# Kernel optimization log

Measured on AMD Instinct MI355X. Metric: run time of the kernel, lower is better.

## Reference

```python
import jax, jax.numpy as jnp
import numpy as np

K_NEIGHBOURS = 40  # includes self; self is dropped after top-k


def setup_inputs() -> dict:
    key = jax.random.key(0)
    ks = jax.random.split(key, 4)
    B, V, F_in = 4, 4096, 64
    P, S, F_out = 64, 4, 64
    x = jax.random.normal(ks[0], (B, V, F_in), dtype=jnp.float32)
    Wf = jax.random.normal(ks[1], (F_in, P), dtype=jnp.float32) / np.sqrt(F_in)
    bf = jnp.zeros((P,), dtype=jnp.float32)
    Ws = jax.random.normal(ks[2], (F_in, S), dtype=jnp.float32) / np.sqrt(F_in)
    bs = jnp.zeros((S,), dtype=jnp.float32)
    Wo = jax.random.normal(ks[3], (F_in + 2 * P, F_out), dtype=jnp.float32) / np.sqrt(F_in + 2 * P)
    bo = jnpp = jnp.zeros((F_out,), dtype=jnp.float32)
    return {"x": x, "Wf": Wf, "bf": bf, "Ws": Ws, "bs": bs, "Wo": Wo, "bo": bo}


def _euclidean_squared(c):
    # c: [B, V, S] -> [B, V, V] squared pairwise distances
    sq = jnp.sum(c * c, axis=-1)  # [B, V]
    d2 = sq[:, :, None] + sq[:, None, :] - 2.0 * jnp.einsum('bvs,bus->bvu', c, c)
    return d2


def reference(x, Wf, bf, Ws, bs, Wo, bo):
    # learned spatial coordinates and propagated features
    coords = x @ Ws + bs            # [B, V, S]
    feats = x @ Wf + bf             # [B, V, P]

    d2 = _euclidean_squared(coords)                 # [B, V, V]
    neg_vals, idx = jax.lax.top_k(-d2, K_NEIGHBOURS)  # closest first (self at 0)
    nbr_idx = idx[:, :, 1:]                         # [B, V, K-1]
    dist = -neg_vals[:, :, 1:]                      # [B, V, K-1] (>= 0)

    # gauss_of_lin(d * 10) = exp(-|10 d|)
    w = jnp.exp(-jnp.abs(dist * 10.0))              # [B, V, K-1]

    # gather neighbour features per batch: [B, V, K-1, P]
    nf = jax.vmap(lambda f, i: f[i])(feats, nbr_idx)
    nf = nf * w[..., None]

    collected = jnp.concatenate([jnp.max(nf, axis=2), jnp.mean(nf, axis=2)], axis=-1)  # [B, V, 2P]
    updated = jnp.concatenate([x, collected], axis=-1)  # [B, V, F_in + 2P]
    return jnp.tanh(updated @ Wo + bo)
```

## Files before the change

### kernel.cpp

```cpp
#include <hip/hip_runtime.h>
#include <cmath>

#define BB  4
#define VV  4096
#define KK  40
#define FIN 64

typedef float v2f __attribute__((ext_vector_type(2)));

__global__ __launch_bounds__(256) void prep_kernel(
    const float* __restrict__ x, const float* __restrict__ Wf,
    const float* __restrict__ bf, const float* __restrict__ Ws,
    const float* __restrict__ bs,
    float* __restrict__ coords, float* __restrict__ sq,
    float* __restrict__ feats)
{
    int lane = threadIdx.x & 63;
    int wid  = threadIdx.x >> 6;
    int row0 = (blockIdx.x * 4 + wid) * 4;
    const float* xr = x + (size_t)row0 * FIN;

    float a0 = 0.f, a1 = 0.f, a2 = 0.f, a3 = 0.f;
    #pragma unroll 8
    for (int k = 0; k < FIN; ++k) {
        float wf = Wf[k * 64 + lane];
        a0 = fmaf(xr[k],        wf, a0);
        a1 = fmaf(xr[64  + k],  wf, a1);
        a2 = fmaf(xr[128 + k],  wf, a2);
        a3 = fmaf(xr[192 + k],  wf, a3);
    }
    float bfl = bf[lane];
    feats[(size_t)(row0 + 0) * 64 + lane] = a0 + bfl;
    feats[(size_t)(row0 + 1) * 64 + lane] = a1 + bfl;
    feats[(size_t)(row0 + 2) * 64 + lane] = a2 + bfl;
    feats[(size_t)(row0 + 3) * 64 + lane] = a3 + bfl;

    int r  = lane >> 4;
    int s  = (lane >> 2) & 3;
    int kc = lane & 3;
    const float* xrr = x + (size_t)(row0 + r) * FIN + kc * 16;
    const float* wsr = Ws + kc * 16 * 4 + s;
    float c = 0.f;
    #pragma unroll
    for (int k = 0; k < 16; ++k)
        c = fmaf(xrr[k], wsr[k * 4], c);
    c += __shfl_xor(c, 1, 64);
    c += __shfl_xor(c, 2, 64);
    float val = c + bs[s];
    if ((lane & 3) == 0) coords[(size_t)(row0 + r) * 4 + s] = val;
    float p = val * val;
    p += __shfl_xor(p, 4, 64);
    p += __shfl_xor(p, 8, 64);
    if ((lane & 15) == 0) sq[row0 + r] = p;
}

__device__ __forceinline__ unsigned umed3(unsigned a, unsigned b, unsigned c)
{
    unsigned d;
    asm("v_med3_u32 %0, %1, %2, %3" : "=v"(d) : "v"(a), "v"(b), "v"(c));
    return d;
}

__device__ __forceinline__ int cnt_lt4(unsigned m0, unsigned m1,
                                       unsigned m2, unsigned m3,
                                       unsigned cand)
{
    return (int)__popcll(__ballot(m0 < cand))
         + (int)__popcll(__ballot(m1 < cand))
         + (int)__popcll(__ballot(m2 < cand))
         + (int)__popcll(__ballot(m3 < cand));
}

__device__ __forceinline__ unsigned select_thresh(unsigned m0, unsigned m1,
                                                  unsigned m2, unsigned m3)
{
    unsigned M = 0u;
    #pragma unroll
    for (int bit = 30; bit >= 12; --bit) {
        unsigned cand = M | (1u << bit);
        if (cnt_lt4(m0, m1, m2, m3, cand) <= 39) M = cand;
    }
    unsigned Msel = M | 0xFFFu;
    if (cnt_lt4(m0, m1, m2, m3, M + 4096u) != 40) {
        #pragma unroll
        for (int bit = 11; bit >= 0; --bit) {
            unsigned cand = M | (1u << bit);
            if (cnt_lt4(m0, m1, m2, m3, cand) <= 39) M = cand;
        }
        Msel = M;
    }
    return Msel;
}

__device__ __forceinline__ void compact4(unsigned m0, unsigned m1,
                                         unsigned m2, unsigned m3,
                                         unsigned Msel, uint2* dst)
{
    unsigned mn = m0;
    #pragma unroll
    for (int off = 32; off >= 1; off >>= 1) {
        unsigned o = __shfl_xor(mn, off, 64);
        mn = o < mn ? o : mn;
    }
    int base = 0;
    unsigned kk = m0;
    #pragma unroll
    for (int i = 0; i < 4; ++i) {
        bool pred = (kk <= Msel) && (kk != mn);
        unsigned long long mask = __ballot(pred);
        unsigned pos = (unsigned)base +
            __builtin_amdgcn_mbcnt_hi((unsigned)(mask >> 32),
                __builtin_amdgcn_mbcnt_lo((unsigned)mask, 0u));
        if (pred) {
            float d2a = __uint_as_float(kk & 0xFFFFF000u);
            float w   = __expf(-10.f * d2a);
            dst[pos] = make_uint2((kk & 4095u) << 8, __float_as_uint(w));
        }
        base += (int)__popcll(mask);
        kk = (i == 0) ? m1 : (i == 1) ? m2 : m3;
    }
}

__global__ __launch_bounds__(128) void gravnet_kernel(
    const float* __restrict__ x, const float* __restrict__ coords,
    const float* __restrict__ sq, const float* __restrict__ feats,
    const float* __restrict__ Wo, const float* __restrict__ bo,
    float* __restrict__ out)
{
    int lane = threadIdx.x & 63;
    int w    = threadIdx.x >> 6;
    int half = w;
    int qb   = blockIdx.x * 4;
    int b    = qb >> 12;
    int v0   = qb & (VV - 1);

    __shared__ __align__(16) char smem[8192];
    uint4* s_mrg  = (uint4*)smem;
    uint2* s_nb   = (uint2*)smem;
    v2f*   s_updp = (v2f*)(smem + 4 * KK * 8);

    const float4* cb  = (const float4*)(coords + (size_t)b * VV * 4);
    const float*  sqb = sq + (size_t)b * VV;

    float4 cq0 = cb[v0],     cq1 = cb[v0 + 1];
    float4 cq2 = cb[v0 + 2], cq3 = cb[v0 + 3];
    v2f nxA = (v2f){-2.f * cq0.x, -2.f * cq1.x};
    v2f nyA = (v2f){-2.f * cq0.y, -2.f * cq1.y};
    v2f nzA = (v2f){-2.f * cq0.z, -2.f * cq1.z};
    v2f nwA = (v2f){-2.f * cq0.w, -2.f * cq1.w};
    v2f hsA = (v2f){sqb[v0], sqb[v0 + 1]};
    v2f nxB = (v2f){-2.f * cq2.x, -2.f * cq3.x};
    v2f nyB = (v2f){-2.f * cq2.y, -2.f * cq3.y};
    v2f nzB = (v2f){-2.f * cq2.z, -2.f * cq3.z};
    v2f nwB = (v2f){-2.f * cq2.w, -2.f * cq3.w};
    v2f hsB = (v2f){sqb[v0 + 2], sqb[v0 + 3]};
    v2f zero = (v2f){0.f, 0.f};

    unsigned k00 = ~0u, k01 = ~0u, k02 = ~0u, k03 = ~0u;
    unsigned k10 = ~0u, k11 = ~0u, k12 = ~0u, k13 = ~0u;
    unsigned k20 = ~0u, k21 = ~0u, k22 = ~0u, k23 = ~0u;
    unsigned k30 = ~0u, k31 = ~0u, k32 = ~0u, k33 = ~0u;

    int i0 = half * 32;
    #pragma unroll 4
    for (int i = i0; i < i0 + 32; ++i) {
        int u = i * 64 + lane;
        float4 cu = cb[u];
        float squ = sqb[u];
        v2f accA = hsA + (v2f){squ, squ};
        accA = __builtin_elementwise_fma(nxA, (v2f){cu.x, cu.x}, accA);
        accA = __builtin_elementwise_fma(nyA, (v2f){cu.y, cu.y}, accA);
        accA = __builtin_elementwise_fma(nzA, (v2f){cu.z, cu.z}, accA);
        accA = __builtin_elementwise_fma(nwA, (v2f){cu.w, cu.w}, accA);
        v2f accB = hsB + (v2f){squ, squ};
        accB = __builtin_elementwise_fma(nxB, (v2f){cu.x, cu.x}, accB);
        accB = __builtin_elementwise_fma(nyB, (v2f){cu.y, cu.y}, accB);
        accB = __builtin_elementwise_fma(nzB, (v2f){cu.z, cu.z}, accB);
        accB = __builtin_elementwise_fma(nwB, (v2f){cu.w, cu.w}, accB);
        accA = __builtin_elementwise_max(accA, zero);
        accB = __builtin_elementwise_max(accB, zero);

        {
            unsigned k = (__float_as_uint(accA.x) & 0xFFFFF000u) | (unsigned)u;
            unsigned n1 = umed3(k00, k01, k);
            unsigned n2 = umed3(k01, k02, k);
            unsigned n3 = umed3(k02, k03, k);
            k00 = min(k00, k); k01 = n1; k02 = n2; k03 = n3;
        }
        {
            unsigned k = (__float_as_uint(accA.y) & 0xFFFFF000u) | (unsigned)u;
            unsigned n1 = umed3(k10, k11, k);
            unsigned n2 = umed3(k11, k12, k);
            unsigned n3 = umed3(k12, k13, k);
            k10 = min(k10, k); k11 = n1; k12 = n2; k13 = n3;
        }
        {
            unsigned k = (__float_as_uint(accB.x) & 0xFFFFF000u) | (unsigned)u;
            unsigned n1 = umed3(k20, k21, k);
            unsigned n2 = umed3(k21, k22, k);
            unsigned n3 = umed3(k22, k23, k);
            k20 = min(k20, k); k21 = n1; k22 = n2; k23 = n3;
        }
        {
            unsigned k = (__float_as_uint(accB.y) & 0xFFFFF000u) | (unsigned)u;
            unsigned n1 = umed3(k30, k31, k);
            unsigned n2 = umed3(k31, k32, k);
            unsigned n3 = umed3(k32, k33, k);
            k30 = min(k30, k); k31 = n1; k32 = n2; k33 = n3;
        }
    }

    s_mrg[(w * 4 + 0) * 64 + lane] = make_uint4(k00, k01, k02, k03);
    s_mrg[(w * 4 + 1) * 64 + lane] = make_uint4(k10, k11, k12, k13);
    s_mrg[(w * 4 + 2) * 64 + lane] = make_uint4(k20, k21, k22, k23);
    s_mrg[(w * 4 + 3) * 64 + lane] = make_uint4(k30, k31, k32, k33);
    __syncthreads();

    int p   = w ^ 1;
    int lq0 = w * 2;
    uint4 pb0 = s_mrg[(p * 4 + lq0)     * 64 + lane];
    uint4 pb1 = s_mrg[(p * 4 + lq0 + 1) * 64 + lane];
    unsigned oa0 = w ? k20 : k00, oa1 = w ? k21 : k01;
    unsigned oa2 = w ? k22 : k02, oa3 = w ? k23 : k03;
    unsigned ob0 = w ? k30 : k10, ob1 = w ? k31 : k11;
    unsigned ob2 = w ? k32 : k12, ob3 = w ? k33 : k13;
    __syncthreads();

    unsigned d0 = min(oa0, pb0.w), d1 = min(oa1, pb0.z);
    unsigned d2 = min(oa2, pb0.y), d3 = min(oa3, pb0.x);
    unsigned A0 = min(d0, d3), A3 = max(d0, d3);
    unsigned e0 = min(ob0, pb1.w), e1 = min(ob1, pb1.z);
    unsigned e2 = min(ob2, pb1.y), e3 = min(ob3, pb1.x);
    unsigned B0 = min(e0, e3), B3 = max(e0, e3);

    int s0 = w * 2, s1 = w * 2 + 1;
    compact4(A0, d1, d2, A3, select_thresh(A0, d1, d2, A3), &s_nb[s0 * KK]);
    compact4(B0, e1, e2, B3, select_thresh(B0, e1, e2, B3), &s_nb[s1 * KK]);

    const float* fb  = feats + (size_t)b * VV * 64;
    const char*  fbl = (const char*)(fb + lane);
    float vmax0 = -INFINITY, vsum0 = 0.f, vmax1 = -INFINITY, vsum1 = 0.f;
    #pragma unroll 6
    for (int j = 0; j < KK - 1; ++j) {
        uint2 n0 = s_nb[s0 * KK + j];
        uint2 n1 = s_nb[s1 * KK + j];
        float f0 = *(const float*)(fbl + n0.x);
        float f1 = *(const float*)(fbl + n1.x);
        float g0 = __uint_as_float(n0.y) * f0;
        float g1 = __uint_as_float(n1.y) * f1;
        vmax0 = fmaxf(vmax0, g0); vsum0 += g0;
        vmax1 = fmaxf(vmax1, g1); vsum1 += g1;
    }

    int q0g = qb + lq0, q1g = qb + lq0 + 1;
    s_updp[w * 192 + lane]       = (v2f){x[(size_t)q0g * 64 + lane],
                                         x[(size_t)q1g * 64 + lane]};
    s_updp[w * 192 + 64  + lane] = (v2f){vmax0, vmax1};
    s_updp[w * 192 + 128 + lane] = (v2f){vsum0 * (1.0f / 39.0f),
                                         vsum1 * (1.0f / 39.0f)};

    float bol = bo[lane];
    v2f accp = (v2f){bol, bol};
    #pragma unroll 4
    for (int j4 = 0; j4 < 48; ++j4) {
        float wo0 = Wo[(j4 * 4 + 0) * 64 + lane];
        float wo1 = Wo[(j4 * 4 + 1) * 64 + lane];
        float wo2 = Wo[(j4 * 4 + 2) * 64 + lane];
        float wo3 = Wo[(j4 * 4 + 3) * 64 + lane];
        float4 r0 = *(const float4*)&s_updp[w * 192 + j4 * 4];
        float4 r1 = *(const float4*)&s_updp[w * 192 + j4 * 4 + 2];
        accp = __builtin_elementwise_fma((v2f){r0.x, r0.y}, (v2f){wo0, wo0}, accp);
        accp = __builtin_elementwise_fma((v2f){r0.z, r0.w}, (v2f){wo1, wo1}, accp);
        accp = __builtin_elementwise_fma((v2f){r1.x, r1.y}, (v2f){wo2, wo2}, accp);
        accp = __builtin_elementwise_fma((v2f){r1.z, r1.w}, (v2f){wo3, wo3}, accp);
    }
    float e0t = __expf(2.f * accp.x);
    float e1t = __expf(2.f * accp.y);
    out[(size_t)q0g * 64 + lane] = 1.f - __fdividef(2.f, e0t + 1.f);
    out[(size_t)q1g * 64 + lane] = 1.f - __fdividef(2.f, e1t + 1.f);
}

extern "C" void kernel_launch(void* const* d_in, const int* in_sizes, int n_in,
                              void* d_out, int out_size, void* d_ws, size_t ws_size,
                              hipStream_t stream)
{
    (void)in_sizes; (void)n_in; (void)out_size; (void)ws_size;
    const float* x  = (const float*)d_in[0];
    const float* Wf = (const float*)d_in[1];
    const float* bf = (const float*)d_in[2];
    const float* Ws = (const float*)d_in[3];
    const float* bs = (const float*)d_in[4];
    const float* Wo = (const float*)d_in[5];
    const float* bo = (const float*)d_in[6];
    float* out = (float*)d_out;

    float* coords = (float*)d_ws;
    float* sq     = coords + (size_t)BB * VV * 4;
    float* feats  = sq + (size_t)BB * VV;

    prep_kernel<<<BB * VV / 16, 256, 0, stream>>>(x, Wf, bf, Ws, bs,
                                                  coords, sq, feats);
    gravnet_kernel<<<BB * VV / 4, 128, 0, stream>>>(x, coords, sq, feats,
                                                    Wo, bo, out);
}
```

Baseline: 127.4 us.

## Split output projection into register-blocked GEMM kernel and recompute squared norms inline

The Wo projection and tanh move out of the kNN/aggregation kernel into a separate out_gemm kernel. Each wave there handles 8 rows, so each loaded Wo value is reused across more rows. The aggregation kernel now writes the max and mean features to global buffers, with the max staged in the output buffer. Squared coordinate norms are recomputed from the coords instead of being stored and loaded, which removes the sq array. The cost is an extra kernel launch and a global write and read of the intermediate max/mean features.

```diff
diff --git a/kernel.cpp b/kernel.cpp
--- a/kernel.cpp
+++ b/kernel.cpp
@@ -12,8 +12,7 @@
     const float* __restrict__ x, const float* __restrict__ Wf,
     const float* __restrict__ bf, const float* __restrict__ Ws,
     const float* __restrict__ bs,
-    float* __restrict__ coords, float* __restrict__ sq,
-    float* __restrict__ feats)
+    float* __restrict__ coords, float* __restrict__ feats)
 {
     int lane = threadIdx.x & 63;
     int wid  = threadIdx.x >> 6;
@@ -48,10 +47,6 @@
     c += __shfl_xor(c, 2, 64);
     float val = c + bs[s];
     if ((lane & 3) == 0) coords[(size_t)(row0 + r) * 4 + s] = val;
-    float p = val * val;
-    p += __shfl_xor(p, 4, 64);
-    p += __shfl_xor(p, 8, 64);
-    if ((lane & 15) == 0) sq[row0 + r] = p;
 }
 
 __device__ __forceinline__ unsigned umed3(unsigned a, unsigned b, unsigned c)
@@ -122,38 +117,41 @@
 }
 
 __global__ __launch_bounds__(128) void gravnet_kernel(
-    const float* __restrict__ x, const float* __restrict__ coords,
-    const float* __restrict__ sq, const float* __restrict__ feats,
-    const float* __restrict__ Wo, const float* __restrict__ bo,
-    float* __restrict__ out)
+    const float* __restrict__ coords, const float* __restrict__ feats,
+    float* __restrict__ mxp, float* __restrict__ mnp)
 {
     int lane = threadIdx.x & 63;
     int w    = threadIdx.x >> 6;
-    int half = w;
     int qb   = blockIdx.x * 4;
     int b    = qb >> 12;
     int v0   = qb & (VV - 1);
 
     __shared__ __align__(16) char smem[8192];
-    uint4* s_mrg  = (uint4*)smem;
-    uint2* s_nb   = (uint2*)smem;
-    v2f*   s_updp = (v2f*)(smem + 4 * KK * 8);
-
-    const float4* cb  = (const float4*)(coords + (size_t)b * VV * 4);
-    const float*  sqb = sq + (size_t)b * VV;
+    uint4* s_mrg = (uint4*)smem;
+    uint2* s_nb  = (uint2*)smem;
+
+    const float4* cb = (const float4*)(coords + (size_t)b * VV * 4);
 
     float4 cq0 = cb[v0],     cq1 = cb[v0 + 1];
     float4 cq2 = cb[v0 + 2], cq3 = cb[v0 + 3];
+    float sv0 = fmaf(cq0.w, cq0.w, fmaf(cq0.z, cq0.z,
+                fmaf(cq0.y, cq0.y, cq0.x * cq0.x)));
+    float sv1 = fmaf(cq1.w, cq1.w, fmaf(cq1.z, cq1.z,
+                fmaf(cq1.y, cq1.y, cq1.x * cq1.x)));
+    float sv2 = fmaf(cq2.w, cq2.w, fmaf(cq2.z, cq2.z,
+                fmaf(cq2.y, cq2.y, cq2.x * cq2.x)));
+    float sv3 = fmaf(cq3.w, cq3.w, fmaf(cq3.z, cq3.z,
+                fmaf(cq3.y, cq3.y, cq3.x * cq3.x)));
     v2f nxA = (v2f){-2.f * cq0.x, -2.f * cq1.x};
     v2f nyA = (v2f){-2.f * cq0.y, -2.f * cq1.y};
     v2f nzA = (v2f){-2.f * cq0.z, -2.f * cq1.z};
     v2f nwA = (v2f){-2.f * cq0.w, -2.f * cq1.w};
-    v2f hsA = (v2f){sqb[v0], sqb[v0 + 1]};
+    v2f hsA = (v2f){sv0, sv1};
     v2f nxB = (v2f){-2.f * cq2.x, -2.f * cq3.x};
     v2f nyB = (v2f){-2.f * cq2.y, -2.f * cq3.y};
     v2f nzB = (v2f){-2.f * cq2.z, -2.f * cq3.z};
     v2f nwB = (v2f){-2.f * cq2.w, -2.f * cq3.w};
-    v2f hsB = (v2f){sqb[v0 + 2], sqb[v0 + 3]};
+    v2f hsB = (v2f){sv2, sv3};
     v2f zero = (v2f){0.f, 0.f};
 
     unsigned k00 = ~0u, k01 = ~0u, k02 = ~0u, k03 = ~0u;
@@ -161,12 +159,13 @@
     unsigned k20 = ~0u, k21 = ~0u, k22 = ~0u, k23 = ~0u;
     unsigned k30 = ~0u, k31 = ~0u, k32 = ~0u, k33 = ~0u;
 
-    int i0 = half * 32;
+    int i0 = w * 32;
     #pragma unroll 4
     for (int i = i0; i < i0 + 32; ++i) {
         int u = i * 64 + lane;
         float4 cu = cb[u];
-        float squ = sqb[u];
+        float squ = fmaf(cu.w, cu.w, fmaf(cu.z, cu.z,
+                    fmaf(cu.y, cu.y, cu.x * cu.x)));
         v2f accA = hsA + (v2f){squ, squ};
         accA = __builtin_elementwise_fma(nxA, (v2f){cu.x, cu.x}, accA);
         accA = __builtin_elementwise_fma(nyA, (v2f){cu.y, cu.y}, accA);
@@ -253,31 +252,73 @@
     }
 
     int q0g = qb + lq0, q1g = qb + lq0 + 1;
-    s_updp[w * 192 + lane]       = (v2f){x[(size_t)q0g * 64 + lane],
-                                         x[(size_t)q1g * 64 + lane]};
-    s_updp[w * 192 + 64  + lane] = (v2f){vmax0, vmax1};
-    s_updp[w * 192 + 128 + lane] = (v2f){vsum0 * (1.0f / 39.0f),
-                                         vsum1 * (1.0f / 39.0f)};
-
+    mxp[(size_t)q0g * 64 + lane] = vmax0;
+    mnp[(size_t)q0g * 64 + lane] = vsum0 * (1.0f / 39.0f);
+    mxp[(size_t)q1g * 64 + lane] = vmax1;
+    mnp[(size_t)q1g * 64 + lane] = vsum1 * (1.0f / 39.0f);
+}
+
+__global__ __launch_bounds__(128) void out_gemm(
+    const float* __restrict__ x, const float* __restrict__ mx,
+    const float* __restrict__ mn, const float* __restrict__ Wo,
+    const float* __restrict__ bo, float* __restrict__ out)
+{
+    int lane = threadIdx.x & 63;
+    int w    = threadIdx.x >> 6;
+    int r0   = blockIdx.x * 16 + w * 8;
     float bol = bo[lane];
-    v2f accp = (v2f){bol, bol};
-    #pragma unroll 4
-    for (int j4 = 0; j4 < 48; ++j4) {
-        float wo0 = Wo[(j4 * 4 + 0) * 64 + lane];
-        float wo1 = Wo[(j4 * 4 + 1) * 64 + lane];
-        float wo2 = Wo[(j4 * 4 + 2) * 64 + lane];
-        float wo3 = Wo[(j4 * 4 + 3) * 64 + lane];
-        float4 r0 = *(const float4*)&s_updp[w * 192 + j4 * 4];
-        float4 r1 = *(const float4*)&s_updp[w * 192 + j4 * 4 + 2];
-        accp = __builtin_elementwise_fma((v2f){r0.x, r0.y}, (v2f){wo0, wo0}, accp);
-        accp = __builtin_elementwise_fma((v2f){r0.z, r0.w}, (v2f){wo1, wo1}, accp);
-        accp = __builtin_elementwise_fma((v2f){r1.x, r1.y}, (v2f){wo2, wo2}, accp);
-        accp = __builtin_elementwise_fma((v2f){r1.z, r1.w}, (v2f){wo3, wo3}, accp);
-    }
-    float e0t = __expf(2.f * accp.x);
-    float e1t = __expf(2.f * accp.y);
-    out[(size_t)q0g * 64 + lane] = 1.f - __fdividef(2.f, e0t + 1.f);
-    out[(size_t)q1g * 64 + lane] = 1.f - __fdividef(2.f, e1t + 1.f);
+    float a0 = bol, a1 = bol, a2 = bol, a3 = bol;
+    float a4 = bol, a5 = bol, a6 = bol, a7 = bol;
+
+    const float* segs[3] = { x, mx, mn };
+    #pragma unroll
+    for (int s = 0; s < 3; ++s) {
+        const float* up  = segs[s] + (size_t)r0 * 64;
+        const float* wop = Wo + s * 64 * 64 + lane;
+        #pragma unroll 4
+        for (int k4 = 0; k4 < 16; ++k4) {
+            float4 u0 = *(const float4*)(up + 0 * 64 + k4 * 4);
+            float4 u1 = *(const float4*)(up + 1 * 64 + k4 * 4);
+            float4 u2 = *(const float4*)(up + 2 * 64 + k4 * 4);
+            float4 u3 = *(const float4*)(up + 3 * 64 + k4 * 4);
+            float4 u4 = *(const float4*)(up + 4 * 64 + k4 * 4);
+            float4 u5 = *(const float4*)(up + 5 * 64 + k4 * 4);
+            float4 u6 = *(const float4*)(up + 6 * 64 + k4 * 4);
+            float4 u7 = *(const float4*)(up + 7 * 64 + k4 * 4);
+            float wo0 = wop[(k4 * 4 + 0) * 64];
+            float wo1 = wop[(k4 * 4 + 1) * 64];
+            float wo2 = wop[(k4 * 4 + 2) * 64];
+            float wo3 = wop[(k4 * 4 + 3) * 64];
+            a0 = fmaf(u0.x, wo0, a0); a0 = fmaf(u0.y, wo1, a0);
+            a0 = fmaf(u0.z, wo2, a0); a0 = fmaf(u0.w, wo3, a0);
+            a1 = fmaf(u1.x, wo0, a1); a1 = fmaf(u1.y, wo1, a1);
+            a1 = fmaf(u1.z, wo2, a1); a1 = fmaf(u1.w, wo3, a1);
+            a2 = fmaf(u2.x, wo0, a2); a2 = fmaf(u2.y, wo1, a2);
+            a2 = fmaf(u2.z, wo2, a2); a2 = fmaf(u2.w, wo3, a2);
+            a3 = fmaf(u3.x, wo0, a3); a3 = fmaf(u3.y, wo1, a3);
+            a3 = fmaf(u3.z, wo2, a3); a3 = fmaf(u3.w, wo3, a3);
+            a4 = fmaf(u4.x, wo0, a4); a4 = fmaf(u4.y, wo1, a4);
+            a4 = fmaf(u4.z, wo2, a4); a4 = fmaf(u4.w, wo3, a4);
+            a5 = fmaf(u5.x, wo0, a5); a5 = fmaf(u5.y, wo1, a5);
+            a5 = fmaf(u5.z, wo2, a5); a5 = fmaf(u5.w, wo3, a5);
+            a6 = fmaf(u6.x, wo0, a6); a6 = fmaf(u6.y, wo1, a6);
+            a6 = fmaf(u6.z, wo2, a6); a6 = fmaf(u6.w, wo3, a6);
+            a7 = fmaf(u7.x, wo0, a7); a7 = fmaf(u7.y, wo1, a7);
+            a7 = fmaf(u7.z, wo2, a7); a7 = fmaf(u7.w, wo3, a7);
+        }
+    }
+    float e0 = __expf(2.f * a0), e1 = __expf(2.f * a1);
+    float e2 = __expf(2.f * a2), e3 = __expf(2.f * a3);
+    float e4 = __expf(2.f * a4), e5 = __expf(2.f * a5);
+    float e6 = __expf(2.f * a6), e7 = __expf(2.f * a7);
+    out[(size_t)(r0 + 0) * 64 + lane] = 1.f - __fdividef(2.f, e0 + 1.f);
+    out[(size_t)(r0 + 1) * 64 + lane] = 1.f - __fdividef(2.f, e1 + 1.f);
+    out[(size_t)(r0 + 2) * 64 + lane] = 1.f - __fdividef(2.f, e2 + 1.f);
+    out[(size_t)(r0 + 3) * 64 + lane] = 1.f - __fdividef(2.f, e3 + 1.f);
+    out[(size_t)(r0 + 4) * 64 + lane] = 1.f - __fdividef(2.f, e4 + 1.f);
+    out[(size_t)(r0 + 5) * 64 + lane] = 1.f - __fdividef(2.f, e5 + 1.f);
+    out[(size_t)(r0 + 6) * 64 + lane] = 1.f - __fdividef(2.f, e6 + 1.f);
+    out[(size_t)(r0 + 7) * 64 + lane] = 1.f - __fdividef(2.f, e7 + 1.f);
 }
 
 extern "C" void kernel_launch(void* const* d_in, const int* in_sizes, int n_in,
@@ -295,11 +336,12 @@
     float* out = (float*)d_out;
 
     float* coords = (float*)d_ws;
-    float* sq     = coords + (size_t)BB * VV * 4;
-    float* feats  = sq + (size_t)BB * VV;
+    float* feats  = coords + (size_t)BB * VV * 4;
+    float* mn     = feats + (size_t)BB * VV * 64;
+    float* mx     = out;
 
     prep_kernel<<<BB * VV / 16, 256, 0, stream>>>(x, Wf, bf, Ws, bs,
-                                                  coords, sq, feats);
-    gravnet_kernel<<<BB * VV / 4, 128, 0, stream>>>(x, coords, sq, feats,
-                                                    Wo, bo, out);
-}
+                                                  coords, feats);
+    gravnet_kernel<<<BB * VV / 4, 128, 0, stream>>>(coords, feats, mx, mn);
+    out_gemm<<<BB * VV / 16, 128, 0, stream>>>(x, mx, mn, Wo, bo, out);
+}
```

Result: slower. 147.5 us (+15.8%).

## Recompute squared norms inline, stage x in LDS, double query block size

Applied to the files above, without the earlier changes.

The separate squared-norm buffer is dropped: norms are recomputed from coordinates inside the distance loop, trading extra FMAs per candidate for one less global load stream. The prep kernel stages x rows in shared memory and computes four output columns per thread using float4 weight loads. The main kernel now runs 8 queries per 256-thread block (two independent quads) instead of 4 per 128 threads. Recomputing norms can change rounding slightly versus the stored values, and the diff leaves unseen code that indexes shared buffers by wave, which may not be updated consistently for the new quad layout.

```diff
diff --git a/kernel.cpp b/kernel.cpp
--- a/kernel.cpp
+++ b/kernel.cpp
@@ -12,28 +12,42 @@
     const float* __restrict__ x, const float* __restrict__ Wf,
     const float* __restrict__ bf, const float* __restrict__ Ws,
     const float* __restrict__ bs,
-    float* __restrict__ coords, float* __restrict__ sq,
-    float* __restrict__ feats)
-{
-    int lane = threadIdx.x & 63;
-    int wid  = threadIdx.x >> 6;
-    int row0 = (blockIdx.x * 4 + wid) * 4;
-    const float* xr = x + (size_t)row0 * FIN;
-
-    float a0 = 0.f, a1 = 0.f, a2 = 0.f, a3 = 0.f;
-    #pragma unroll 8
-    for (int k = 0; k < FIN; ++k) {
-        float wf = Wf[k * 64 + lane];
-        a0 = fmaf(xr[k],        wf, a0);
-        a1 = fmaf(xr[64  + k],  wf, a1);
-        a2 = fmaf(xr[128 + k],  wf, a2);
-        a3 = fmaf(xr[192 + k],  wf, a3);
-    }
-    float bfl = bf[lane];
-    feats[(size_t)(row0 + 0) * 64 + lane] = a0 + bfl;
-    feats[(size_t)(row0 + 1) * 64 + lane] = a1 + bfl;
-    feats[(size_t)(row0 + 2) * 64 + lane] = a2 + bfl;
-    feats[(size_t)(row0 + 3) * 64 + lane] = a3 + bfl;
+    float* __restrict__ coords, float* __restrict__ feats)
+{
+    int tid  = threadIdx.x;
+    int lane = tid & 63;
+    int w    = tid >> 6;
+    int row0 = blockIdx.x * 16 + w * 4;
+
+    __shared__ __align__(16) float sx[16 * 68];
+
+    #pragma unroll
+    for (int i = 0; i < 4; ++i)
+        sx[(w * 4 + i) * 68 + lane] = x[(size_t)(row0 + i) * 64 + lane];
+
+    int rgrp = lane >> 4;
+    int colg = lane & 15;
+    const float4* Wf4 = (const float4*)Wf;
+    float4 acc = make_float4(0.f, 0.f, 0.f, 0.f);
+    #pragma unroll 4
+    for (int k4 = 0; k4 < 16; ++k4) {
+        float4 u  = *(const float4*)&sx[(w * 4 + rgrp) * 68 + k4 * 4];
+        float4 w0 = Wf4[(k4 * 4 + 0) * 16 + colg];
+        float4 w1 = Wf4[(k4 * 4 + 1) * 16 + colg];
+        float4 w2 = Wf4[(k4 * 4 + 2) * 16 + colg];
+        float4 w3 = Wf4[(k4 * 4 + 3) * 16 + colg];
+        acc.x = fmaf(u.x, w0.x, acc.x); acc.y = fmaf(u.x, w0.y, acc.y);
+        acc.z = fmaf(u.x, w0.z, acc.z); acc.w = fmaf(u.x, w0.w, acc.w);
+        acc.x = fmaf(u.y, w1.x, acc.x); acc.y = fmaf(u.y, w1.y, acc.y);
+        acc.z = fmaf(u.y, w1.z, acc.z); acc.w = fmaf(u.y, w1.w, acc.w);
+        acc.x = fmaf(u.z, w2.x, acc.x); acc.y = fmaf(u.z, w2.y, acc.y);
+        acc.z = fmaf(u.z, w2.z, acc.z); acc.w = fmaf(u.z, w2.w, acc.w);
+        acc.x = fmaf(u.w, w3.x, acc.x); acc.y = fmaf(u.w, w3.y, acc.y);
+        acc.z = fmaf(u.w, w3.z, acc.z); acc.w = fmaf(u.w, w3.w, acc.w);
+    }
+    float4 bf4 = ((const float4*)bf)[colg];
+    acc.x += bf4.x; acc.y += bf4.y; acc.z += bf4.z; acc.w += bf4.w;
+    *(float4*)&feats[(size_t)(row0 + rgrp) * 64 + colg * 4] = acc;
 
     int r  = lane >> 4;
     int s  = (lane >> 2) & 3;
@@ -48,10 +62,6 @@
     c += __shfl_xor(c, 2, 64);
     float val = c + bs[s];
     if ((lane & 3) == 0) coords[(size_t)(row0 + r) * 4 + s] = val;
-    float p = val * val;
-    p += __shfl_xor(p, 4, 64);
-    p += __shfl_xor(p, 8, 64);
-    if ((lane & 15) == 0) sq[row0 + r] = p;
 }
 
 __device__ __forceinline__ unsigned umed3(unsigned a, unsigned b, unsigned c)
@@ -121,39 +131,46 @@
     }
 }
 
-__global__ __launch_bounds__(128) void gravnet_kernel(
+__global__ __launch_bounds__(256) void gravnet_kernel(
     const float* __restrict__ x, const float* __restrict__ coords,
-    const float* __restrict__ sq, const float* __restrict__ feats,
-    const float* __restrict__ Wo, const float* __restrict__ bo,
-    float* __restrict__ out)
+    const float* __restrict__ feats, const float* __restrict__ Wo,
+    const float* __restrict__ bo, float* __restrict__ out)
 {
     int lane = threadIdx.x & 63;
     int w    = threadIdx.x >> 6;
-    int half = w;
-    int qb   = blockIdx.x * 4;
-    int b    = qb >> 12;
+    int quad = w >> 1;
+    int half = w & 1;
+    int qb   = blockIdx.x * 8 + quad * 4;
+    int b    = (blockIdx.x * 8) >> 12;
     int v0   = qb & (VV - 1);
 
-    __shared__ __align__(16) char smem[8192];
+    __shared__ __align__(16) char smem[16384];
     uint4* s_mrg  = (uint4*)smem;
     uint2* s_nb   = (uint2*)smem;
-    v2f*   s_updp = (v2f*)(smem + 4 * KK * 8);
-
-    const float4* cb  = (const float4*)(coords + (size_t)b * VV * 4);
-    const float*  sqb = sq + (size_t)b * VV;
+    v2f*   s_updp = (v2f*)(smem + 8 * KK * 8);
+
+    const float4* cb = (const float4*)(coords + (size_t)b * VV * 4);
 
     float4 cq0 = cb[v0],     cq1 = cb[v0 + 1];
     float4 cq2 = cb[v0 + 2], cq3 = cb[v0 + 3];
+    float sv0 = fmaf(cq0.w, cq0.w, fmaf(cq0.z, cq0.z,
+                fmaf(cq0.y, cq0.y, cq0.x * cq0.x)));
+    float sv1 = fmaf(cq1.w, cq1.w, fmaf(cq1.z, cq1.z,
+                fmaf(cq1.y, cq1.y, cq1.x * cq1.x)));
+    float sv2 = fmaf(cq2.w, cq2.w, fmaf(cq2.z, cq2.z,
+                fmaf(cq2.y, cq2.y, cq2.x * cq2.x)));
+    float sv3 = fmaf(cq3.w, cq3.w, fmaf(cq3.z, cq3.z,
+                fmaf(cq3.y, cq3.y, cq3.x * cq3.x)));
     v2f nxA = (v2f){-2.f * cq0.x, -2.f * cq1.x};
     v2f nyA = (v2f){-2.f * cq0.y, -2.f * cq1.y};
     v2f nzA = (v2f){-2.f * cq0.z, -2.f * cq1.z};
     v2f nwA = (v2f){-2.f * cq0.w, -2.f * cq1.w};
-    v2f hsA = (v2f){sqb[v0], sqb[v0 + 1]};
+    v2f hsA = (v2f){sv0, sv1};
     v2f nxB = (v2f){-2.f * cq2.x, -2.f * cq3.x};
     v2f nyB = (v2f){-2.f * cq2.y, -2.f * cq3.y};
     v2f nzB = (v2f){-2.f * cq2.z, -2.f * cq3.z};
     v2f nwB = (v2f){-2.f * cq2.w, -2.f * cq3.w};
-    v2f hsB = (v2f){sqb[v0 + 2], sqb[v0 + 3]};
+    v2f hsB = (v2f){sv2, sv3};
     v2f zero = (v2f){0.f, 0.f};
 
     unsigned k00 = ~0u, k01 = ~0u, k02 = ~0u, k03 = ~0u;
@@ -166,7 +183,8 @@
     for (int i = i0; i < i0 + 32; ++i) {
         int u = i * 64 + lane;
         float4 cu = cb[u];
-        float squ = sqb[u];
+        float squ = fmaf(cu.w, cu.w, fmaf(cu.z, cu.z,
+                    fmaf(cu.y, cu.y, cu.x * cu.x)));
         v2f accA = hsA + (v2f){squ, squ};
         accA = __builtin_elementwise_fma(nxA, (v2f){cu.x, cu.x}, accA);
         accA = __builtin_elementwise_fma(nyA, (v2f){cu.y, cu.y}, accA);
@@ -217,13 +235,13 @@
     __syncthreads();
 
     int p   = w ^ 1;
-    int lq0 = w * 2;
+    int lq0 = half * 2;
     uint4 pb0 = s_mrg[(p * 4 + lq0)     * 64 + lane];
     uint4 pb1 = s_mrg[(p * 4 + lq0 + 1) * 64 + lane];
-    unsigned oa0 = w ? k20 : k00, oa1 = w ? k21 : k01;
-    unsigned oa2 = w ? k22 : k02, oa3 = w ? k23 : k03;
-    unsigned ob0 = w ? k30 : k10, ob1 = w ? k31 : k11;
-    unsigned ob2 = w ? k32 : k12, ob3 = w ? k33 : k13;
+    unsigned oa0 = half ? k20 : k00, oa1 = half ? k21 : k01;
+    unsigned oa2 = half ? k22 : k02, oa3 = half ? k23 : k03;
+    unsigned ob0 = half ? k30 : k10, ob1 = half ? k31 : k11;
+    unsigned ob2 = half ? k32 : k12, ob3 = half ? k33 : k13;
     __syncthreads();
 
     unsigned d0 = min(oa0, pb0.w), d1 = min(oa1, pb0.z);
@@ -295,11 +313,10 @@
     float* out = (float*)d_out;
 
     float* coords = (float*)d_ws;
-    float* sq     = coords + (size_t)BB * VV * 4;
-    float* feats  = sq + (size_t)BB * VV;
+    float* feats  = coords + (size_t)BB * VV * 4;
 
     prep_kernel<<<BB * VV / 16, 256, 0, stream>>>(x, Wf, bf, Ws, bs,
-                                                  coords, sq, feats);
-    gravnet_kernel<<<BB * VV / 4, 128, 0, stream>>>(x, coords, sq, feats,
+                                                  coords, feats);
+    gravnet_kernel<<<BB * VV / 8, 256, 0, stream>>>(x, coords, feats,
                                                     Wo, bo, out);
 }
```

After: 127.3 us. About the same (-0.1%).
